# Optimization experiments

Hardware: AMD Instinct MI355X
Metric: run time of the kernel (lower is better)

Reference implementation:

```python
import jax, jax.numpy as jnp
import numpy as np

H = 1024   # dim_hidden
K = 64     # number of tasks
T_STEPS = 2048


def setup_inputs() -> dict:
    key = jax.random.key(0)
    ks = jax.random.split(key, 12)
    s = 1.0 / np.sqrt(H)
    inp = {
        "z":    jax.random.normal(ks[0], (H,), jnp.float32),
        "Wih":  jax.random.normal(ks[1], (4 * H, H), jnp.float32) * s,
        "Whh":  jax.random.normal(ks[2], (4 * H, H), jnp.float32) * s,
        "b_ih": jax.random.normal(ks[3], (4 * H,), jnp.float32) * s,
        "b_hh": jax.random.normal(ks[4], (4 * H,), jnp.float32) * s,
        "W1":   jax.random.normal(ks[5], (32, H), jnp.float32) * s,
        "b1":   jax.random.normal(ks[6], (32,), jnp.float32) * s,
        "W2":   jax.random.normal(ks[7], (32, 32), jnp.float32) * (1.0 / np.sqrt(32)),
        "b2":   jax.random.normal(ks[8], (32,), jnp.float32) * (1.0 / np.sqrt(32)),
        "W3":   jax.random.normal(ks[9], (K, 32), jnp.float32) * (1.0 / np.sqrt(32)),
        "b3":   jax.random.normal(ks[10], (K,), jnp.float32) * (1.0 / np.sqrt(32)),
        "T":    T_STEPS,
    }
    return inp


def reference(z, Wih, Whh, b_ih, b_hh, W1, b1, W2, b2, W3, b3, T):
    h0 = jnp.zeros_like(z)
    c0 = jnp.zeros_like(z)

    def cell(carry, _):
        x, h, c = carry  # x is the LSTM input this step (z first, then fed-back h)
        gates = x @ Wih.T + b_ih + h @ Whh.T + b_hh  # (4H,), torch gate order i,f,g,o
        i, f, g, o = jnp.split(gates, 4)
        c_new = jax.nn.sigmoid(f) * c + jax.nn.sigmoid(i) * jnp.tanh(g)
        h_new = jax.nn.sigmoid(o) * jnp.tanh(c_new)
        # torch LSTM output y == h_new; fed back as next input
        return (h_new, h_new, c_new), h_new

    _, hs = jax.lax.scan(cell, (z, h0, c0), None, length=T)  # hs: (T, H)

    # MLP applied per timestep, vectorized over T
    a = jax.nn.relu(hs @ W1.T + b1)
    a = jax.nn.relu(a @ W2.T + b2)
    rewards = a @ W3.T + b3  # (T, K)
    return rewards
```

## Files before the change

### kernel.cpp

```cpp
#include <hip/hip_runtime.h>
#include <math.h>

#define H        1024
#define TSTEPS   2048
#define NWG      64
#define NT       1024
#define PAD      68
#define SENT     0xFFFFFFFFu

typedef unsigned u32x4 __attribute__((ext_vector_type(4)));

__device__ __forceinline__ u32x4 load16_agent(const unsigned* p) {
    u32x4 r;
    asm volatile("global_load_dwordx4 %0, %1, off sc1\n\ts_waitcnt vmcnt(0)"
                 : "=v"(r) : "v"(p) : "memory");
    return r;
}

__device__ __forceinline__ float fsig(float x)   { return 1.0f / (1.0f + __expf(-x)); }
__device__ __forceinline__ float ftanh_(float x) { return 1.0f - 2.0f / (__expf(2.0f * x) + 1.0f); }

__global__ __launch_bounds__(NT, 1) void lstm_persistent(
    const float* __restrict__ z,   const float* __restrict__ Wih,
    const float* __restrict__ Whh, const float* __restrict__ b_ih,
    const float* __restrict__ b_hh,
    const float* __restrict__ W1,  const float* __restrict__ b1,
    const float* __restrict__ W2,  const float* __restrict__ b2,
    const float* __restrict__ W3,  const float* __restrict__ b3,
    float* __restrict__ out, float* __restrict__ hs)
{
    __shared__ __align__(16) float hbuf[2][16 * PAD];
    __shared__ __align__(16) float mlp_buf[4][16 * PAD];
    __shared__ float gates_lds[64];
    __shared__ float a1_lds[4][32];
    __shared__ float a2_lds[4][32];

    const int tid = threadIdx.x;
    const int wg  = blockIdx.x;
    const int r   = tid >> 4;
    const int seg = tid & 15;
    const int g   = r >> 4;
    const int e   = r & 15;
    const int grow = g * H + wg * 16 + e;
    const float bias = b_ih[grow] + b_hh[grow];

    if (tid < 256) {
        float4 zv = *(const float4*)(z + tid * 4);
        *(float4*)(&hbuf[0][(tid >> 4) * PAD + (tid & 15) * 4]) = zv;
    }
    __syncthreads();

    float4 wreg[16];
    float s0 = 0.f, s1 = 0.f, s2 = 0.f, s3 = 0.f;
    const float* wihp = Wih + (size_t)grow * H + seg * 64;
    const float* whhp = Whh + (size_t)grow * H + seg * 64;
#pragma unroll
    for (int k = 0; k < 16; ++k) {
        float4 a  = *(const float4*)(wihp + 4 * k);
        float4 b  = *(const float4*)(whhp + 4 * k);
        float4 zz = *(const float4*)(&hbuf[0][seg * PAD + 4 * k]);
        float d = a.x * zz.x + a.y * zz.y + a.z * zz.z + a.w * zz.w;
        if ((k & 3) == 0) s0 += d; else if ((k & 3) == 1) s1 += d;
        else if ((k & 3) == 2) s2 += d; else s3 += d;
        wreg[k] = make_float4(a.x + b.x, a.y + b.y, a.z + b.z, a.w + b.w);
    }
    {
        float acc = (s0 + s1) + (s2 + s3);
        acc += __shfl_xor(acc, 1); acc += __shfl_xor(acc, 2);
        acc += __shfl_xor(acc, 4); acc += __shfl_xor(acc, 8);
        if (seg == 0) gates_lds[r] = acc + bias;
    }
    __syncthreads();

    float c_reg = 0.f;
    if (tid >= 960 && tid < 976) {
        int el = tid - 960;
        float gi = gates_lds[el],      gg = gates_lds[32 + el], go = gates_lds[48 + el];
        float c = fsig(gi) * ftanh_(gg);
        float h = fsig(go) * ftanh_(c);
        c_reg = c;
        __hip_atomic_store((unsigned*)hs + wg * 16 + el, __float_as_uint(h),
                           __ATOMIC_RELAXED, __HIP_MEMORY_SCOPE_AGENT);
    }

    for (int t = 1; t < TSTEPS; ++t) {
        if (tid < 256) {
            const unsigned* p = (const unsigned*)hs + (size_t)(t - 1) * H + tid * 4;
            u32x4 v;
            for (;;) {
                v = load16_agent(p);
                if (v.x != SENT && v.y != SENT && v.z != SENT && v.w != SENT) break;
            }
            float* dst = &hbuf[t & 1][(tid >> 4) * PAD + (tid & 15) * 4];
            dst[0] = __uint_as_float(v.x); dst[1] = __uint_as_float(v.y);
            dst[2] = __uint_as_float(v.z); dst[3] = __uint_as_float(v.w);
        }
        __syncthreads();

        const float* hb = &hbuf[t & 1][seg * PAD];
        float q0 = 0.f, q1 = 0.f, q2 = 0.f, q3 = 0.f;
#pragma unroll
        for (int k = 0; k < 16; ++k) {
            float4 h4 = *(const float4*)(hb + 4 * k);
            float4 wv = wreg[k];
            float d = wv.x * h4.x + wv.y * h4.y + wv.z * h4.z + wv.w * h4.w;
            if ((k & 3) == 0) q0 += d; else if ((k & 3) == 1) q1 += d;
            else if ((k & 3) == 2) q2 += d; else q3 += d;
        }
        float a2 = (q0 + q1) + (q2 + q3);
        a2 += __shfl_xor(a2, 1); a2 += __shfl_xor(a2, 2);
        a2 += __shfl_xor(a2, 4); a2 += __shfl_xor(a2, 8);
        if (seg == 0) gates_lds[r] = a2 + bias;
        __syncthreads();

        if (tid >= 960 && tid < 976) {
            int el = tid - 960;
            float gi = gates_lds[el],      gf = gates_lds[16 + el];
            float gg = gates_lds[32 + el], go = gates_lds[48 + el];
            float cn = fsig(gf) * c_reg + fsig(gi) * ftanh_(gg);
            float hn = fsig(go) * ftanh_(cn);
            c_reg = cn;
            __hip_atomic_store((unsigned*)(hs + (size_t)t * H) + wg * 16 + el,
                               __float_as_uint(hn),
                               __ATOMIC_RELAXED, __HIP_MEMORY_SCOPE_AGENT);
        }
    }

    const int local = tid & 255;
    const int grp   = tid >> 8;
    const int row32 = local >> 3;
    const int sub   = local & 7;
    for (int ti = 0; ti < 8; ++ti) {
        int t = wg * 32 + ti * 4 + grp;
        __syncthreads();
        {
            const unsigned* p = (const unsigned*)hs + (size_t)t * H + local * 4;
            u32x4 v;
            for (;;) {
                v = load16_agent(p);
                if (v.x != SENT && v.y != SENT && v.z != SENT && v.w != SENT) break;
            }
            float* dst = &mlp_buf[grp][(local >> 4) * PAD + (local & 15) * 4];
            dst[0] = __uint_as_float(v.x); dst[1] = __uint_as_float(v.y);
            dst[2] = __uint_as_float(v.z); dst[3] = __uint_as_float(v.w);
        }
        __syncthreads();

        float acc1 = 0.f;
        const float* w1p = W1 + (size_t)row32 * H + sub * 128;
#pragma unroll
        for (int k = 0; k < 32; ++k) {
            float4 wv = *(const float4*)(w1p + 4 * k);
            int c = sub * 128 + 4 * k;
            float4 h4 = *(const float4*)(&mlp_buf[grp][(c >> 6) * PAD + (c & 63)]);
            acc1 += wv.x * h4.x + wv.y * h4.y + wv.z * h4.z + wv.w * h4.w;
        }
        acc1 += __shfl_xor(acc1, 1); acc1 += __shfl_xor(acc1, 2); acc1 += __shfl_xor(acc1, 4);
        if (sub == 0) a1_lds[grp][row32] = fmaxf(acc1 + b1[row32], 0.f);
        __syncthreads();

        if (local < 32) {
            float a = 0.f;
#pragma unroll
            for (int k = 0; k < 32; ++k) a += W2[local * 32 + k] * a1_lds[grp][k];
            a2_lds[grp][local] = fmaxf(a + b2[local], 0.f);
        }
        __syncthreads();

        if (local < 64) {
            float a = 0.f;
#pragma unroll
            for (int k = 0; k < 32; ++k) a += W3[local * 32 + k] * a2_lds[grp][k];
            out[(size_t)t * 64 + local] = a + b3[local];
        }
    }
}

extern "C" void kernel_launch(void* const* d_in, const int* in_sizes, int n_in,
                              void* d_out, int out_size, void* d_ws, size_t ws_size,
                              hipStream_t stream) {
    const float* z    = (const float*)d_in[0];
    const float* Wih  = (const float*)d_in[1];
    const float* Whh  = (const float*)d_in[2];
    const float* b_ih = (const float*)d_in[3];
    const float* b_hh = (const float*)d_in[4];
    const float* W1   = (const float*)d_in[5];
    const float* b1   = (const float*)d_in[6];
    const float* W2   = (const float*)d_in[7];
    const float* b2   = (const float*)d_in[8];
    const float* W3   = (const float*)d_in[9];
    const float* b3   = (const float*)d_in[10];
    float* out = (float*)d_out;

    float* hs = (float*)d_ws;

    hipMemsetAsync(hs, 0xFF, (size_t)TSTEPS * H * sizeof(float), stream);
    hipLaunchKernelGGL(lstm_persistent, dim3(NWG), dim3(NT), 0, stream,
                       z, Wih, Whh, b_ih, b_hh, W1, b1, W2, b2, W3, b3,
                       out, hs);
}
```

Baseline: 4.120 ms.

## Map each wave to one hidden unit so gates combine via shuffles without barrier

```diff
diff --git a/kernel.cpp b/kernel.cpp
--- a/kernel.cpp
+++ b/kernel.cpp
@@ -31,17 +31,17 @@
 {
     __shared__ __align__(16) float hbuf[2][16 * PAD];
     __shared__ __align__(16) float mlp_buf[4][16 * PAD];
-    __shared__ float gates_lds[64];
     __shared__ float a1_lds[4][32];
     __shared__ float a2_lds[4][32];
 
-    const int tid = threadIdx.x;
-    const int wg  = blockIdx.x;
-    const int r   = tid >> 4;
-    const int seg = tid & 15;
-    const int g   = r >> 4;
-    const int e   = r & 15;
-    const int grow = g * H + wg * 16 + e;
+    const int tid  = threadIdx.x;
+    const int wg   = blockIdx.x;
+    const int wave = tid >> 6;
+    const int lane = tid & 63;
+    const int g    = lane >> 4;
+    const int seg  = lane & 15;
+    const int E    = wg * 16 + wave;
+    const int grow = g * H + E;
     const float bias = b_ih[grow] + b_hh[grow];
 
     if (tid < 256) {
@@ -64,23 +64,19 @@
         else if ((k & 3) == 2) s2 += d; else s3 += d;
         wreg[k] = make_float4(a.x + b.x, a.y + b.y, a.z + b.z, a.w + b.w);
     }
+    float c_reg;
     {
         float acc = (s0 + s1) + (s2 + s3);
         acc += __shfl_xor(acc, 1); acc += __shfl_xor(acc, 2);
         acc += __shfl_xor(acc, 4); acc += __shfl_xor(acc, 8);
-        if (seg == 0) gates_lds[r] = acc + bias;
-    }
-    __syncthreads();
-
-    float c_reg = 0.f;
-    if (tid >= 960 && tid < 976) {
-        int el = tid - 960;
-        float gi = gates_lds[el],      gg = gates_lds[32 + el], go = gates_lds[48 + el];
-        float c = fsig(gi) * ftanh_(gg);
-        float h = fsig(go) * ftanh_(c);
-        c_reg = c;
-        __hip_atomic_store((unsigned*)hs + wg * 16 + el, __float_as_uint(h),
-                           __ATOMIC_RELAXED, __HIP_MEMORY_SCOPE_AGENT);
+        acc += bias;
+        float sigv = fsig(acc), tanv = ftanh_(acc);
+        float si = __shfl(sigv, 0), tg = __shfl(tanv, 32), so = __shfl(sigv, 48);
+        c_reg = si * tg;
+        float h = so * ftanh_(c_reg);
+        if (lane == 0)
+            __hip_atomic_store((unsigned*)hs + E, __float_as_uint(h),
+                               __ATOMIC_RELAXED, __HIP_MEMORY_SCOPE_AGENT);
     }
 
     for (int t = 1; t < TSTEPS; ++t) {
@@ -110,20 +106,17 @@
         float a2 = (q0 + q1) + (q2 + q3);
         a2 += __shfl_xor(a2, 1); a2 += __shfl_xor(a2, 2);
         a2 += __shfl_xor(a2, 4); a2 += __shfl_xor(a2, 8);
-        if (seg == 0) gates_lds[r] = a2 + bias;
-        __syncthreads();
-
-        if (tid >= 960 && tid < 976) {
-            int el = tid - 960;
-            float gi = gates_lds[el],      gf = gates_lds[16 + el];
-            float gg = gates_lds[32 + el], go = gates_lds[48 + el];
-            float cn = fsig(gf) * c_reg + fsig(gi) * ftanh_(gg);
-            float hn = fsig(go) * ftanh_(cn);
-            c_reg = cn;
-            __hip_atomic_store((unsigned*)(hs + (size_t)t * H) + wg * 16 + el,
+        a2 += bias;
+        float sigv = fsig(a2), tanv = ftanh_(a2);
+        float si = __shfl(sigv, 0),  sf = __shfl(sigv, 16);
+        float tg = __shfl(tanv, 32), so = __shfl(sigv, 48);
+        float cn = sf * c_reg + si * tg;
+        float hn = so * ftanh_(cn);
+        c_reg = cn;
+        if (lane == 0)
+            __hip_atomic_store((unsigned*)(hs + (size_t)t * H) + E,
                                __float_as_uint(hn),
                                __ATOMIC_RELAXED, __HIP_MEMORY_SCOPE_AGENT);
-        }
     }
 
     const int local = tid & 255;
```

After: 7.698 ms. 86.9% more time.
